# Performance work log

Hardware: AMD Instinct MI355X
Metric: run time of the kernel (lower is better)

The kernel has to match this reference:

```python
import jax, jax.numpy as jnp
import numpy as np

B, T, F = 32, 2048, 16
C = F + 1      # input channels (time prepended)
H = 64         # output_dims: latent CDE state size
HH = 64        # hidden_dims: vector-field MLP width
DEPTH = 4      # num_hidden_layers -> DEPTH-1 inner linears
INIT = 64      # intial_dims


def _lin(k, fan_in, shape):
    b = 1.0 / np.sqrt(fan_in)
    return jax.random.uniform(k, shape, jnp.float32, -b, b)


def setup_inputs() -> dict:
    key = jax.random.key(0)
    ks = jax.random.split(key, 15)
    return {
        "x": jax.random.normal(ks[0], (B, T, F), jnp.float32),
        # z0 initializer MLP: Linear(C,INIT) -> ReLU -> Linear(INIT,H)
        "wi1": _lin(ks[1], C, (C, INIT)), "bi1": _lin(ks[2], C, (INIT,)),
        "wi2": _lin(ks[3], INIT, (INIT, H)), "bi2": _lin(ks[4], INIT, (H,)),
        # CDEFunc
        "w_in": _lin(ks[5], H, (H, HH)), "b_in": _lin(ks[6], H, (HH,)),
        "w_hid": _lin(ks[7], HH, (DEPTH - 1, HH, HH)), "b_hid": _lin(ks[8], HH, (DEPTH - 1, HH)),
        "w_out": _lin(ks[9], HH, (HH, C * H)), "b_out": _lin(ks[10], HH, (C * H,)),
        # output projection Linear(H, F)
        "w_proj": _lin(ks[11], H, (H, F)), "b_proj": _lin(ks[12], H, (F,)),
    }


def _cde_f(z, w_in, b_in, w_hid, b_hid, w_out, b_out):
    # CDEFunc.forward: MLP -> tanh, reshaped to (b, H, C)
    h = jax.nn.relu(z @ w_in + b_in)
    for i in range(w_hid.shape[0]):
        h = jax.nn.relu(h @ w_hid[i] + b_hid[i])
    return jnp.tanh((h @ w_out + b_out).reshape(z.shape[0], H, C))


def _forward(x, wi1, bi1, wi2, bi2, w_in, b_in, w_hid, b_hid, w_out, b_out, w_proj, b_proj):
    b, t_len, _ = x.shape
    t = jnp.arange(t_len, dtype=x.dtype)
    xa = jnp.concatenate([jnp.broadcast_to(t[None, :, None], (b, t_len, 1)), x], axis=-1)  # (b,T,C)

    # Hermite cubic with backward differences (torchcde): knot derivs are backward
    # diffs with the first repeated; on interval i (h=1):
    #   X'(s) = d_i + 2*c_i*s + 3*e_i*s^2,  c_i = 3*dx - 2*d_i - d_{i+1},  e_i = -2*dx + d_i + d_{i+1}
    diffs = xa[:, 1:] - xa[:, :-1]                      # (b,T-1,C)
    d = jnp.concatenate([diffs[:, :1], diffs], axis=1)  # (b,T,C)
    di, dip1 = d[:, :-1], d[:, 1:]
    cc = 3.0 * diffs - 2.0 * di - dip1
    ee = -2.0 * diffs + di + dip1

    def deriv(s):
        return di + (2.0 * s) * cc + (3.0 * s * s) * ee  # (b,T-1,C)

    # torchdiffeq 'rk4' = 3/8-rule: evals at s = 0, 1/3, 2/3, 1 within each unit interval
    xdots = jnp.stack([deriv(0.0), deriv(1.0 / 3.0), deriv(2.0 / 3.0), deriv(1.0)], axis=0)
    xdots = jnp.moveaxis(xdots, 2, 0)  # (T-1, 4, b, C)

    z0 = jax.nn.relu(xa[:, 0] @ wi1 + bi1) @ wi2 + bi2  # (b,H)

    def g(z, xd):
        f = _cde_f(z, w_in, b_in, w_hid, b_hid, w_out, b_out)  # (b,H,C)
        return jnp.einsum('bhc,bc->bh', f, xd)

    def step(z, xd4):
        k1 = g(z, xd4[0])
        k2 = g(z + k1 / 3.0, xd4[1])
        k3 = g(z + (k2 - k1 / 3.0), xd4[2])
        k4 = g(z + (k1 - k2 + k3), xd4[3])
        zn = z + (k1 + 3.0 * (k2 + k3) + k4) * 0.125
        return zn, zn

    _, zs = jax.lax.scan(step, z0, xdots)                # (T-1,b,H)
    z_T = jnp.moveaxis(jnp.concatenate([z0[None], zs], axis=0), 0, 1)  # (b,T,H)

    # act -> dropout (eval: identity) -> output_layer
    out = jax.nn.gelu(z_T, approximate=False) @ w_proj + b_proj        # (b,T,F)
    return z_T, out


def reference(x, wi1, bi1, wi2, bi2, w_in, b_in, w_hid, b_hid, w_out, b_out, w_proj, b_proj):
    z_T, out = _forward(x, wi1, bi1, wi2, bi2, w_in, b_in, w_hid, b_hid, w_out, b_out, w_proj, b_proj)
    not_mask = jnp.zeros((x.shape[0], x.shape[1]), dtype=bool)  # mask='all_true' (eval mode)
    return z_T, out, not_mask
```

## Files before the change

kernel.cpp:

```cpp
#include <hip/hip_runtime.h>
#include <math.h>

#define BB 32
#define TT 2048
#define FF 16
#define CC 17
#define HH 64

typedef float v2f __attribute__((ext_vector_type(2)));
typedef float v4f __attribute__((ext_vector_type(4)));
typedef unsigned v4u __attribute__((ext_vector_type(4)));
typedef _Float16 h2 __attribute__((ext_vector_type(2)));

__device__ __forceinline__ float rl(float v, int lane) {
    return __int_as_float(__builtin_amdgcn_readlane(__float_as_int(v), lane));
}
__device__ __forceinline__ unsigned rlu(unsigned v, int lane) {
    return (unsigned)__builtin_amdgcn_readlane((int)v, lane);
}
__device__ __forceinline__ float uf(float v) {
    return __int_as_float(__builtin_amdgcn_readfirstlane(__float_as_int(v)));
}
__device__ __forceinline__ float ftanh(float x) {
    float e = __builtin_amdgcn_exp2f(x * 2.88539008177792681472f);
    return 1.0f - 2.0f * __builtin_amdgcn_rcpf(e + 1.0f);
}
__device__ __forceinline__ float fdot2u(unsigned a, unsigned b, float c) {
    return __builtin_amdgcn_fdot2(__builtin_bit_cast(h2, a),
                                  __builtin_bit_cast(h2, b), c, false);
}
__device__ __forceinline__ unsigned packw(float a, float b) {
    h2 p; p.x = (_Float16)(a * 256.0f); p.y = (_Float16)(b * 256.0f);
    return __builtin_bit_cast(unsigned, p);
}
__device__ __forceinline__ void bar_lds() {
    asm volatile("s_waitcnt lgkmcnt(0)\n\ts_barrier" ::: "memory");
}
#define PIN(v) asm volatile("" : "+v"(v))

__attribute__((amdgpu_waves_per_eu(2, 2)))
__launch_bounds__(512)
__global__ void ncde_main(const float* __restrict__ x,
                          const float* __restrict__ wi1, const float* __restrict__ bi1,
                          const float* __restrict__ wi2, const float* __restrict__ bi2,
                          const float* __restrict__ w_in, const float* __restrict__ b_in,
                          const float* __restrict__ w_hid, const float* __restrict__ b_hid,
                          const float* __restrict__ w_out, const float* __restrict__ b_out,
                          float* __restrict__ zT)
{
    const int b   = blockIdx.x;
    const int tid = threadIdx.x;
    const int w   = tid >> 6;
    const int l   = tid & 63;

    __shared__ __align__(16) unsigned h2b[32];
    __shared__ __align__(16) unsigned hbuf[32];
    __shared__ float pgqt[64][20];

    const int nc    = (w >= 2) ? ((w < 7) ? 3 : 2) : 0;
    const int cbase = (w < 7) ? 3 * (w - 2) : 15;
    const int pcol  = (w >= 2) ? ((w - 2 + (l >> 3)) % 6) : 0;

    unsigned wreg[96];
    #pragma unroll
    for (int i = 0; i < 96; ++i) wreg[i] = 0u;
    float bA = 0.f, bB = 0.f, bC = 0.f;
    if (w == 0) {
        #pragma unroll
        for (int p = 0; p < 32; ++p) {
            wreg[p]      = packw(w_in[(2 * p) * HH + l],          w_in[(2 * p + 1) * HH + l]);
            wreg[32 + p] = packw(w_hid[(0 * HH + 2 * p) * HH + l], w_hid[(0 * HH + 2 * p + 1) * HH + l]);
        }
        bA = b_in[l];  bB = b_hid[l];
    } else if (w == 1) {
        #pragma unroll
        for (int p = 0; p < 32; ++p) {
            wreg[p]      = packw(w_hid[(1 * HH + 2 * p) * HH + l], w_hid[(1 * HH + 2 * p + 1) * HH + l]);
            wreg[32 + p] = packw(w_hid[(2 * HH + 2 * p) * HH + l], w_hid[(2 * HH + 2 * p + 1) * HH + l]);
        }
        bA = b_hid[HH + l];  bB = b_hid[2 * HH + l];
    } else {
        #pragma unroll
        for (int i = 0; i < 3; ++i) {
            if (i < nc) {
                int c = cbase + i;
                #pragma unroll
                for (int p = 0; p < 32; ++p)
                    wreg[32 * i + p] = packw(w_out[(2 * p) * (CC * HH) + l * CC + c],
                                             w_out[(2 * p + 1) * (CC * HH) + l * CC + c]);
            }
        }
        bA = b_out[l * CC + cbase];
        bB = b_out[l * CC + cbase + 1];
        if (nc == 3) bC = b_out[l * CC + cbase + 2];
    }
    #pragma unroll
    for (int i = 0; i < 96; ++i) PIN(wreg[i]);
    PIN(bA); PIN(bB); PIN(bC);

    float z;
    {
        float h0 = bi1[l];
        #pragma unroll
        for (int c = 1; c < CC; ++c)
            h0 = fmaf(x[(size_t)b * TT * FF + (c - 1)], wi1[c * HH + l], h0);
        h0 = fmaxf(h0, 0.0f);
        z = bi2[l];
        #pragma unroll
        for (int k = 0; k < 64; ++k)
            z = fmaf(rl(h0, k), wi2[k * HH + l], z);
    }
    if (w == 7) zT[(size_t)b * TT * HH + l] = z;

    auto packb = [&](float v) -> unsigned {
        float hs = v * 0.00390625f;
        float pr = __shfl_xor(hs, 1);
        float a  = (l & 1) ? pr : hs;
        float bb = (l & 1) ? hs : pr;
        return __builtin_bit_cast(unsigned, __builtin_amdgcn_cvt_pkrtz(a, bb));
    };

    auto LAYER_RL = [&](const unsigned* Wc, float bias, unsigned hp) -> float {
        float a0 = bias, a1 = 0.f, a2 = 0.f, a3 = 0.f;
        #pragma unroll
        for (int p = 0; p < 32; p += 4) {
            unsigned s0 = rlu(hp, 2 * p);
            unsigned s1 = rlu(hp, 2 * p + 2);
            unsigned s2 = rlu(hp, 2 * p + 4);
            unsigned s3 = rlu(hp, 2 * p + 6);
            a0 = fdot2u(s0, Wc[p],     a0);
            a1 = fdot2u(s1, Wc[p + 1], a1);
            a2 = fdot2u(s2, Wc[p + 2], a2);
            a3 = fdot2u(s3, Wc[p + 3], a3);
        }
        return fmaxf((a0 + a1) + (a2 + a3), 0.0f);
    };
    auto LAYER_LDS = [&](const unsigned* Wc, float bias, const unsigned* hs) -> float {
        v4u q0 = *reinterpret_cast<const v4u*>(&hs[0]);
        v4u q1 = *reinterpret_cast<const v4u*>(&hs[4]);
        v4u q2 = *reinterpret_cast<const v4u*>(&hs[8]);
        v4u q3 = *reinterpret_cast<const v4u*>(&hs[12]);
        v4u q4 = *reinterpret_cast<const v4u*>(&hs[16]);
        v4u q5 = *reinterpret_cast<const v4u*>(&hs[20]);
        v4u q6 = *reinterpret_cast<const v4u*>(&hs[24]);
        v4u q7 = *reinterpret_cast<const v4u*>(&hs[28]);
        float a0 = bias, a1 = 0.f, a2 = 0.f, a3 = 0.f;
        a0 = fdot2u(q0.x, Wc[0],  a0); a1 = fdot2u(q0.y, Wc[1],  a1);
        a2 = fdot2u(q0.z, Wc[2],  a2); a3 = fdot2u(q0.w, Wc[3],  a3);
        a0 = fdot2u(q1.x, Wc[4],  a0); a1 = fdot2u(q1.y, Wc[5],  a1);
        a2 = fdot2u(q1.z, Wc[6],  a2); a3 = fdot2u(q1.w, Wc[7],  a3);
        a0 = fdot2u(q2.x, Wc[8],  a0); a1 = fdot2u(q2.y, Wc[9],  a1);
        a2 = fdot2u(q2.z, Wc[10], a2); a3 = fdot2u(q2.w, Wc[11], a3);
        a0 = fdot2u(q3.x, Wc[12], a0); a1 = fdot2u(q3.y, Wc[13], a1);
        a2 = fdot2u(q3.z, Wc[14], a2); a3 = fdot2u(q3.w, Wc[15], a3);
        a0 = fdot2u(q4.x, Wc[16], a0); a1 = fdot2u(q4.y, Wc[17], a1);
        a2 = fdot2u(q4.z, Wc[18], a2); a3 = fdot2u(q4.w, Wc[19], a3);
        a0 = fdot2u(q5.x, Wc[20], a0); a1 = fdot2u(q5.y, Wc[21], a1);
        a2 = fdot2u(q5.z, Wc[22], a2); a3 = fdot2u(q5.w, Wc[23], a3);
        a0 = fdot2u(q6.x, Wc[24], a0); a1 = fdot2u(q6.y, Wc[25], a1);
        a2 = fdot2u(q6.z, Wc[26], a2); a3 = fdot2u(q6.w, Wc[27], a3);
        a0 = fdot2u(q7.x, Wc[28], a0); a1 = fdot2u(q7.y, Wc[29], a1);
        a2 = fdot2u(q7.z, Wc[30], a2); a3 = fdot2u(q7.w, Wc[31], a3);
        return fmaxf((a0 + a1) + (a2 + a3), 0.0f);
    };
    auto DOT32 = [&](const unsigned* Wc, float bias,
                     v4u q0, v4u q1, v4u q2, v4u q3,
                     v4u q4, v4u q5, v4u q6, v4u q7) -> float {
        float a0 = bias, a1 = 0.f, a2 = 0.f, a3 = 0.f;
        a0 = fdot2u(q0.x, Wc[0],  a0); a1 = fdot2u(q0.y, Wc[1],  a1);
        a2 = fdot2u(q0.z, Wc[2],  a2); a3 = fdot2u(q0.w, Wc[3],  a3);
        a0 = fdot2u(q1.x, Wc[4],  a0); a1 = fdot2u(q1.y, Wc[5],  a1);
        a2 = fdot2u(q1.z, Wc[6],  a2); a3 = fdot2u(q1.w, Wc[7],  a3);
        a0 = fdot2u(q2.x, Wc[8],  a0); a1 = fdot2u(q2.y, Wc[9],  a1);
        a2 = fdot2u(q2.z, Wc[10], a2); a3 = fdot2u(q2.w, Wc[11], a3);
        a0 = fdot2u(q3.x, Wc[12], a0); a1 = fdot2u(q3.y, Wc[13], a1);
        a2 = fdot2u(q3.z, Wc[14], a2); a3 = fdot2u(q3.w, Wc[15], a3);
        a0 = fdot2u(q4.x, Wc[16], a0); a1 = fdot2u(q4.y, Wc[17], a1);
        a2 = fdot2u(q4.z, Wc[18], a2); a3 = fdot2u(q4.w, Wc[19], a3);
        a0 = fdot2u(q5.x, Wc[20], a0); a1 = fdot2u(q5.y, Wc[21], a1);
        a2 = fdot2u(q5.z, Wc[22], a2); a3 = fdot2u(q5.w, Wc[23], a3);
        a0 = fdot2u(q6.x, Wc[24], a0); a1 = fdot2u(q6.y, Wc[25], a1);
        a2 = fdot2u(q6.z, Wc[26], a2); a3 = fdot2u(q6.w, Wc[27], a3);
        a0 = fdot2u(q7.x, Wc[28], a0); a1 = fdot2u(q7.y, Wc[29], a1);
        a2 = fdot2u(q7.z, Wc[30], a2); a3 = fdot2u(q7.w, Wc[31], a3);
        return (a0 + a1) + (a2 + a3);
    };

    auto G = [&](float zin, float xd0, float xd1, float xd2) -> float {
        if (w == 0) {
            unsigned hp0 = packb(zin);
            float h1v = LAYER_RL(&wreg[0],  bA, hp0);
            unsigned hp1 = packb(h1v);
            float h2v = LAYER_RL(&wreg[32], bB, hp1);
            unsigned hp2 = packb(h2v);
            if (!(l & 1)) h2b[l >> 1] = hp2;
        }
        bar_lds();
        if (w == 1) {
            float h3v = LAYER_LDS(&wreg[0], bA, h2b);
            unsigned hp3 = packb(h3v);
            float h4v = LAYER_RL(&wreg[32], bB, hp3);
            unsigned hp4 = packb(h4v);
            if (!(l & 1)) hbuf[l >> 1] = hp4;
        }
        bar_lds();
        if (w >= 2) {
            v4u q0 = *reinterpret_cast<const v4u*>(&hbuf[0]);
            v4u q1 = *reinterpret_cast<const v4u*>(&hbuf[4]);
            v4u q2 = *reinterpret_cast<const v4u*>(&hbuf[8]);
            v4u q3 = *reinterpret_cast<const v4u*>(&hbuf[12]);
            v4u q4 = *reinterpret_cast<const v4u*>(&hbuf[16]);
            v4u q5 = *reinterpret_cast<const v4u*>(&hbuf[20]);
            v4u q6 = *reinterpret_cast<const v4u*>(&hbuf[24]);
            v4u q7 = *reinterpret_cast<const v4u*>(&hbuf[28]);
            float u0 = DOT32(&wreg[0],  bA, q0, q1, q2, q3, q4, q5, q6, q7);
            float u1 = DOT32(&wreg[32], bB, q0, q1, q2, q3, q4, q5, q6, q7);
            float pg = ftanh(u0) * xd0 + ftanh(u1) * xd1;
            if (nc == 3) {
                float u2 = DOT32(&wreg[64], bC, q0, q1, q2, q3, q4, q5, q6, q7);
                pg = fmaf(ftanh(u2), xd2, pg);
            }
            pgqt[l][pcol] = pg;
        }
        bar_lds();
        const float* pr = &pgqt[l][0];
        v4f r0 = *reinterpret_cast<const v4f*>(pr);
        v2f r1 = *reinterpret_cast<const v2f*>(pr + 4);
        return ((r0.x + r0.y) + (r0.z + r0.w)) + (r1.x + r1.y);
    };

    const float* xb = x + (size_t)b * TT * FF;
    float xp[3] = {0, 0, 0}, dcv[3] = {0, 0, 0}, dpv[3] = {0, 0, 0};
    #pragma unroll
    for (int i = 0; i < 3; ++i) {
        if (i < nc) {
            int f = cbase + i - 1;
            float v0 = (f < 0) ? 0.f : uf(xb[f]);
            float v1 = (f < 0) ? 0.f : uf(xb[FF + f]);
            dcv[i] = (f < 0) ? 1.0f : (v1 - v0);
            dpv[i] = dcv[i];
            xp[i]  = v1;
        }
    }

    #pragma unroll 1
    for (int t = 0; t < TT - 1; ++t) {
        const float f43 = 4.0f / 3.0f;
        float x2[3] = {0, 0, 0};
        #pragma unroll
        for (int i = 0; i < 3; ++i)
            if (i < nc) x2[i] = dpv[i] + f43 * (dcv[i] - dpv[i]);

        int tn = (t + 2 < TT) ? (t + 2) : (TT - 1);
        float yn[3] = {0, 0, 0};
        #pragma unroll
        for (int i = 0; i < 3; ++i) {
            if (i < nc) {
                int f = cbase + i - 1;
                yn[i] = (f < 0) ? 0.f : uf(xb[tn * FF + f]);
            }
        }

        float k1 = G(z, dpv[0], dpv[1], dpv[2]);
        float k2 = G(z + k1 * (1.0f / 3.0f), dcv[0], dcv[1], dcv[2]);
        float k3 = G(z + (k2 - k1 * (1.0f / 3.0f)), x2[0], x2[1], x2[2]);
        float k4 = G(z + (k1 - k2 + k3), dcv[0], dcv[1], dcv[2]);
        z = z + 0.125f * (k1 + 3.0f * (k2 + k3) + k4);

        if (w == 7) zT[((size_t)b * TT + t + 1) * HH + l] = z;

        #pragma unroll
        for (int i = 0; i < 3; ++i) {
            if (i < nc) {
                int f = cbase + i - 1;
                dpv[i] = dcv[i];
                dcv[i] = (f < 0) ? 1.0f : (yn[i] - xp[i]);
                xp[i]  = yn[i];
            }
        }
    }
}

__global__ void ncde_proj(const float* __restrict__ zT,
                          const float* __restrict__ w_proj, const float* __restrict__ b_proj,
                          float* __restrict__ out, float* __restrict__ mask)
{
    __shared__ float gz[16][64];
    const int blk = blockIdx.x;
    const int tid = threadIdx.x;
    const int r16 = tid >> 4, f = tid & 15;
    const int row0 = blk * 16;

    #pragma unroll
    for (int i = 0; i < 4; ++i) {
        int idx = tid + i * 256;
        int r = idx >> 6, k = idx & 63;
        float zv = zT[(size_t)(row0 + r) * HH + k];
        gz[r][k] = 0.5f * zv * (1.0f + erff(zv * 0.70710678118654752f));
    }
    __syncthreads();

    float acc = b_proj[f];
    #pragma unroll
    for (int k = 0; k < 64; ++k)
        acc = fmaf(gz[r16][k], w_proj[k * FF + f], acc);
    out[(size_t)(row0 + r16) * FF + f] = acc;
    if (f == 0) mask[row0 + r16] = 0.0f;
}

extern "C" void kernel_launch(void* const* d_in, const int* in_sizes, int n_in,
                              void* d_out, int out_size, void* d_ws, size_t ws_size,
                              hipStream_t stream)
{
    (void)in_sizes; (void)n_in; (void)d_ws; (void)ws_size; (void)out_size;
    const float* x      = (const float*)d_in[0];
    const float* wi1    = (const float*)d_in[1];
    const float* bi1    = (const float*)d_in[2];
    const float* wi2    = (const float*)d_in[3];
    const float* bi2    = (const float*)d_in[4];
    const float* w_in   = (const float*)d_in[5];
    const float* b_in   = (const float*)d_in[6];
    const float* w_hid  = (const float*)d_in[7];
    const float* b_hid  = (const float*)d_in[8];
    const float* w_out  = (const float*)d_in[9];
    const float* b_out  = (const float*)d_in[10];
    const float* w_proj = (const float*)d_in[11];
    const float* b_proj = (const float*)d_in[12];

    float* zT   = (float*)d_out;
    float* outp = zT + (size_t)BB * TT * HH;
    float* mask = outp + (size_t)BB * TT * FF;

    ncde_main<<<dim3(BB), dim3(512), 0, stream>>>(
        x, wi1, bi1, wi2, bi2, w_in, b_in, w_hid, b_hid, w_out, b_out, zT);
    ncde_proj<<<dim3((BB * TT) / 16), dim3(256), 0, stream>>>(
        zT, w_proj, b_proj, outp, mask);
}
```

Before: 11.72 ms.

## Run all four MLP layers in wave 0 using AGPR weights, drop a barrier

Wave 0 now computes all four hidden MLP layers, with the last two layers' weights held in accumulation registers (AGPRs). The seven remaining waves share the 17 output columns, with partial-sum reduction widened to 8 slots. This removes one block barrier and one LDS handoff per vector-field evaluation, in exchange for a longer serial chain in wave 0 and possible AGPR-to-VGPR copy costs when reading the weights.

Result: slower. 12.62 ms (+7.7%).

```diff
diff --git a/kernel.cpp b/kernel.cpp
--- a/kernel.cpp
+++ b/kernel.cpp
@@ -36,7 +36,8 @@
 __device__ __forceinline__ void bar_lds() {
     asm volatile("s_waitcnt lgkmcnt(0)\n\ts_barrier" ::: "memory");
 }
-#define PIN(v) asm volatile("" : "+v"(v))
+#define PIN(v)  asm volatile("" : "+v"(v))
+#define PINA(v) asm volatile("" : "+a"(v))
 
 __attribute__((amdgpu_waves_per_eu(2, 2)))
 __launch_bounds__(512)
@@ -53,32 +54,32 @@
     const int w   = tid >> 6;
     const int l   = tid & 63;
 
-    __shared__ __align__(16) unsigned h2b[32];
     __shared__ __align__(16) unsigned hbuf[32];
     __shared__ float pgqt[64][20];
 
-    const int nc    = (w >= 2) ? ((w < 7) ? 3 : 2) : 0;
-    const int cbase = (w < 7) ? 3 * (w - 2) : 15;
-    const int pcol  = (w >= 2) ? ((w - 2 + (l >> 3)) % 6) : 0;
-
-    unsigned wreg[96];
-    #pragma unroll
-    for (int i = 0; i < 96; ++i) wreg[i] = 0u;
-    float bA = 0.f, bB = 0.f, bC = 0.f;
+    const int nc    = (w == 0) ? 0 : ((w <= 3) ? 3 : 2);
+    const int cbase = (w == 0) ? 0 : ((w <= 3) ? 3 * (w - 1) : 9 + 2 * (w - 4));
+    const int pcol  = (w >= 1) ? ((w - 1 + (l >> 3)) % 7) : 0;
+
+    unsigned wregV[96];
+    unsigned wregA[64];
+    #pragma unroll
+    for (int i = 0; i < 96; ++i) wregV[i] = 0u;
+    #pragma unroll
+    for (int i = 0; i < 64; ++i) wregA[i] = 0u;
+    float bA = 0.f, bB = 0.f, bC = 0.f, bD = 0.f;
     if (w == 0) {
         #pragma unroll
         for (int p = 0; p < 32; ++p) {
-            wreg[p]      = packw(w_in[(2 * p) * HH + l],          w_in[(2 * p + 1) * HH + l]);
-            wreg[32 + p] = packw(w_hid[(0 * HH + 2 * p) * HH + l], w_hid[(0 * HH + 2 * p + 1) * HH + l]);
-        }
-        bA = b_in[l];  bB = b_hid[l];
-    } else if (w == 1) {
-        #pragma unroll
-        for (int p = 0; p < 32; ++p) {
-            wreg[p]      = packw(w_hid[(1 * HH + 2 * p) * HH + l], w_hid[(1 * HH + 2 * p + 1) * HH + l]);
-            wreg[32 + p] = packw(w_hid[(2 * HH + 2 * p) * HH + l], w_hid[(2 * HH + 2 * p + 1) * HH + l]);
-        }
-        bA = b_hid[HH + l];  bB = b_hid[2 * HH + l];
+            wregV[p]      = packw(w_in[(2 * p) * HH + l],           w_in[(2 * p + 1) * HH + l]);
+            wregV[32 + p] = packw(w_hid[(0 * HH + 2 * p) * HH + l],  w_hid[(0 * HH + 2 * p + 1) * HH + l]);
+            wregA[p]      = packw(w_hid[(1 * HH + 2 * p) * HH + l],  w_hid[(1 * HH + 2 * p + 1) * HH + l]);
+            wregA[32 + p] = packw(w_hid[(2 * HH + 2 * p) * HH + l],  w_hid[(2 * HH + 2 * p + 1) * HH + l]);
+        }
+        bA = b_in[l];
+        bB = b_hid[l];
+        bC = b_hid[HH + l];
+        bD = b_hid[2 * HH + l];
     } else {
         #pragma unroll
         for (int i = 0; i < 3; ++i) {
@@ -86,8 +87,8 @@
                 int c = cbase + i;
                 #pragma unroll
                 for (int p = 0; p < 32; ++p)
-                    wreg[32 * i + p] = packw(w_out[(2 * p) * (CC * HH) + l * CC + c],
-                                             w_out[(2 * p + 1) * (CC * HH) + l * CC + c]);
+                    wregV[32 * i + p] = packw(w_out[(2 * p) * (CC * HH) + l * CC + c],
+                                              w_out[(2 * p + 1) * (CC * HH) + l * CC + c]);
             }
         }
         bA = b_out[l * CC + cbase];
@@ -95,8 +96,12 @@
         if (nc == 3) bC = b_out[l * CC + cbase + 2];
     }
     #pragma unroll
-    for (int i = 0; i < 96; ++i) PIN(wreg[i]);
-    PIN(bA); PIN(bB); PIN(bC);
+    for (int i = 0; i < 96; ++i) PIN(wregV[i]);
+    #pragma unroll
+    for (int i = 0; i < 64; ++i) PINA(wregA[i]);
+    PIN(bA); PIN(bB); PIN(bC); PIN(bD);
+
+    if (w == 0) pgqt[l][7] = 0.0f;
 
     float z;
     {
@@ -133,34 +138,6 @@
             a2 = fdot2u(s2, Wc[p + 2], a2);
             a3 = fdot2u(s3, Wc[p + 3], a3);
         }
-        return fmaxf((a0 + a1) + (a2 + a3), 0.0f);
-    };
-    auto LAYER_LDS = [&](const unsigned* Wc, float bias, const unsigned* hs) -> float {
-        v4u q0 = *reinterpret_cast<const v4u*>(&hs[0]);
-        v4u q1 = *reinterpret_cast<const v4u*>(&hs[4]);
-        v4u q2 = *reinterpret_cast<const v4u*>(&hs[8]);
-        v4u q3 = *reinterpret_cast<const v4u*>(&hs[12]);
-        v4u q4 = *reinterpret_cast<const v4u*>(&hs[16]);
-        v4u q5 = *reinterpret_cast<const v4u*>(&hs[20]);
-        v4u q6 = *reinterpret_cast<const v4u*>(&hs[24]);
-        v4u q7 = *reinterpret_cast<const v4u*>(&hs[28]);
-        float a0 = bias, a1 = 0.f, a2 = 0.f, a3 = 0.f;
-        a0 = fdot2u(q0.x, Wc[0],  a0); a1 = fdot2u(q0.y, Wc[1],  a1);
-        a2 = fdot2u(q0.z, Wc[2],  a2); a3 = fdot2u(q0.w, Wc[3],  a3);
-        a0 = fdot2u(q1.x, Wc[4],  a0); a1 = fdot2u(q1.y, Wc[5],  a1);
-        a2 = fdot2u(q1.z, Wc[6],  a2); a3 = fdot2u(q1.w, Wc[7],  a3);
-        a0 = fdot2u(q2.x, Wc[8],  a0); a1 = fdot2u(q2.y, Wc[9],  a1);
-        a2 = fdot2u(q2.z, Wc[10], a2); a3 = fdot2u(q2.w, Wc[11], a3);
-        a0 = fdot2u(q3.x, Wc[12], a0); a1 = fdot2u(q3.y, Wc[13], a1);
-        a2 = fdot2u(q3.z, Wc[14], a2); a3 = fdot2u(q3.w, Wc[15], a3);
-        a0 = fdot2u(q4.x, Wc[16], a0); a1 = fdot2u(q4.y, Wc[17], a1);
-        a2 = fdot2u(q4.z, Wc[18], a2); a3 = fdot2u(q4.w, Wc[19], a3);
-        a0 = fdot2u(q5.x, Wc[20], a0); a1 = fdot2u(q5.y, Wc[21], a1);
-        a2 = fdot2u(q5.z, Wc[22], a2); a3 = fdot2u(q5.w, Wc[23], a3);
-        a0 = fdot2u(q6.x, Wc[24], a0); a1 = fdot2u(q6.y, Wc[25], a1);
-        a2 = fdot2u(q6.z, Wc[26], a2); a3 = fdot2u(q6.w, Wc[27], a3);
-        a0 = fdot2u(q7.x, Wc[28], a0); a1 = fdot2u(q7.y, Wc[29], a1);
-        a2 = fdot2u(q7.z, Wc[30], a2); a3 = fdot2u(q7.w, Wc[31], a3);
         return fmaxf((a0 + a1) + (a2 + a3), 0.0f);
     };
     auto DOT32 = [&](const unsigned* Wc, float bias,
@@ -188,23 +165,15 @@
 
     auto G = [&](float zin, float xd0, float xd1, float xd2) -> float {
         if (w == 0) {
-            unsigned hp0 = packb(zin);
-            float h1v = LAYER_RL(&wreg[0],  bA, hp0);
-            unsigned hp1 = packb(h1v);
-            float h2v = LAYER_RL(&wreg[32], bB, hp1);
-            unsigned hp2 = packb(h2v);
-            if (!(l & 1)) h2b[l >> 1] = hp2;
+            unsigned hp = packb(zin);
+            hp = packb(LAYER_RL(&wregV[0],  bA, hp));
+            hp = packb(LAYER_RL(&wregV[32], bB, hp));
+            hp = packb(LAYER_RL(&wregA[0],  bC, hp));
+            hp = packb(LAYER_RL(&wregA[32], bD, hp));
+            if (!(l & 1)) hbuf[l >> 1] = hp;
         }
         bar_lds();
-        if (w == 1) {
-            float h3v = LAYER_LDS(&wreg[0], bA, h2b);
-            unsigned hp3 = packb(h3v);
-            float h4v = LAYER_RL(&wreg[32], bB, hp3);
-            unsigned hp4 = packb(h4v);
-            if (!(l & 1)) hbuf[l >> 1] = hp4;
-        }
-        bar_lds();
-        if (w >= 2) {
+        if (w >= 1) {
             v4u q0 = *reinterpret_cast<const v4u*>(&hbuf[0]);
             v4u q1 = *reinterpret_cast<const v4u*>(&hbuf[4]);
             v4u q2 = *reinterpret_cast<const v4u*>(&hbuf[8]);
@@ -213,11 +182,11 @@
             v4u q5 = *reinterpret_cast<const v4u*>(&hbuf[20]);
             v4u q6 = *reinterpret_cast<const v4u*>(&hbuf[24]);
             v4u q7 = *reinterpret_cast<const v4u*>(&hbuf[28]);
-            float u0 = DOT32(&wreg[0],  bA, q0, q1, q2, q3, q4, q5, q6, q7);
-            float u1 = DOT32(&wreg[32], bB, q0, q1, q2, q3, q4, q5, q6, q7);
+            float u0 = DOT32(&wregV[0],  bA, q0, q1, q2, q3, q4, q5, q6, q7);
+            float u1 = DOT32(&wregV[32], bB, q0, q1, q2, q3, q4, q5, q6, q7);
             float pg = ftanh(u0) * xd0 + ftanh(u1) * xd1;
             if (nc == 3) {
-                float u2 = DOT32(&wreg[64], bC, q0, q1, q2, q3, q4, q5, q6, q7);
+                float u2 = DOT32(&wregV[64], bC, q0, q1, q2, q3, q4, q5, q6, q7);
                 pg = fmaf(ftanh(u2), xd2, pg);
             }
             pgqt[l][pcol] = pg;
@@ -225,8 +194,8 @@
         bar_lds();
         const float* pr = &pgqt[l][0];
         v4f r0 = *reinterpret_cast<const v4f*>(pr);
-        v2f r1 = *reinterpret_cast<const v2f*>(pr + 4);
-        return ((r0.x + r0.y) + (r0.z + r0.w)) + (r1.x + r1.y);
+        v4f r1 = *reinterpret_cast<const v4f*>(pr + 4);
+        return ((r0.x + r0.y) + (r0.z + r0.w)) + ((r1.x + r1.y) + (r1.z + r1.w));
     };
 
     const float* xb = x + (size_t)b * TT * FF;
```
